# Kernel tuning notes

Measured on AMD Instinct MI355X. Metric: run time of the kernel, lower is better.

The kernel has to match this reference:

```python
import jax, jax.numpy as jnp
import numpy as np

B, CIN, H, W = 4, 256, 56, 56
COUT, K = 256, 3
STRIDE, PAD, OG = 1, 1, 1
KK = K * K


def setup_inputs() -> dict:
    key = jax.random.key(0)
    k1, k2, k3, k4 = jax.random.split(key, 4)
    x = jax.random.normal(k1, (B, CIN, H, W), jnp.float32)
    # deformable conv weight [Cout, Cin/groups, K, K]
    weight = jax.random.normal(k2, (COUT, CIN, K, K), jnp.float32) * 0.05
    # offset-predicting 3x3 conv: 2*OG*K*K output channels (small init -> modest offsets)
    off_w = jax.random.normal(k3, (2 * OG * KK, CIN, 3, 3), jnp.float32) * 0.01
    off_b = jax.random.normal(k4, (2 * OG * KK,), jnp.float32) * 0.01
    return {"x": x, "weight": weight, "off_w": off_w, "off_b": off_b}


def _deform_conv(x, weight, off_w, off_b):
    Bn, C, Hh, Ww = x.shape
    # offset = param_generator(x): 3x3 conv, stride 1, pad 1
    offset = jax.lax.conv_general_dilated(
        x, off_w, window_strides=(1, 1), padding=((1, 1), (1, 1)),
        dimension_numbers=("NCHW", "OIHW", "NCHW")) + off_b[None, :, None, None]
    Ho = (Hh + 2 * PAD - K) // STRIDE + 1
    Wo = (Ww + 2 * PAD - K) // STRIDE + 1
    # torchvision layout: [B, OG, KK, (dy,dx), Ho, Wo]
    off = offset.reshape(Bn, OG, KK, 2, Ho, Wo)

    kh = jnp.arange(KK) // K
    kw = jnp.arange(KK) % K
    base_y = (jnp.arange(Ho) * STRIDE - PAD)[None, :, None] + kh[:, None, None]  # [KK,Ho,1]
    base_x = (jnp.arange(Wo) * STRIDE - PAD)[None, None, :] + kw[:, None, None]  # [KK,1,Wo]
    py = base_y[None, None].astype(x.dtype) + off[:, :, :, 0]  # [B,OG,KK,Ho,Wo]
    px = base_x[None, None].astype(x.dtype) + off[:, :, :, 1]

    Cg = C // OG
    xg = x.reshape(Bn, OG, Cg, Hh * Ww)

    def gather(yc, xc, wgt):
        # zero-padded bilinear corner: out-of-bounds samples contribute 0
        valid = (yc >= 0) & (yc < Hh) & (xc >= 0) & (xc < Ww)
        idx = (jnp.clip(yc, 0, Hh - 1) * Ww + jnp.clip(xc, 0, Ww - 1)).reshape(Bn, OG, 1, -1)
        v = jnp.take_along_axis(xg, idx, axis=3)            # [B,OG,Cg,KK*Ho*Wo]
        w = (wgt * valid.astype(wgt.dtype)).reshape(Bn, OG, 1, -1)
        return v * w

    y0 = jnp.floor(py).astype(jnp.int32)
    x0 = jnp.floor(px).astype(jnp.int32)
    ty = py - y0
    tx = px - x0
    sampled = (gather(y0,     x0,     (1 - ty) * (1 - tx))
             + gather(y0,     x0 + 1, (1 - ty) * tx)
             + gather(y0 + 1, x0,     ty * (1 - tx))
             + gather(y0 + 1, x0 + 1, ty * tx))
    sampled = sampled.reshape(Bn, C, KK, Ho, Wo)
    # weighted accumulation: implicit GEMM over (Cin, KK)
    return jnp.einsum("bikhw,oik->bohw", sampled, weight.reshape(COUT, C, KK))


def reference(x, weight, off_w, off_b):
    return _deform_conv(x, weight, off_w, off_b)
```

## Files before the change

### kernel.cpp

```cpp
#include <hip/hip_runtime.h>
#include <hip/hip_bf16.h>

#define B_N   4
#define CIN_  256
#define HH_   56
#define WW_   56
#define COUT_ 256
#define KK_   9
#define HW_   3136
#define KDIM  2304
#define NOFF  (B_N*18*HW_)
#define NOUT  (B_N*COUT_*HW_)

typedef __attribute__((ext_vector_type(8))) short short8;
typedef __attribute__((ext_vector_type(4))) float float4v;

__device__ __forceinline__ short f2bf_bits(float v) {
    union { __hip_bfloat16 h; short s; } u;
    u.h = __float2bfloat16(v);
    return u.s;
}
__device__ __forceinline__ float bfbits2f(short s) {
    union { unsigned u; float f; } u2;
    u2.u = ((unsigned)(unsigned short)s) << 16;
    return u2.f;
}

#define NB_AT  2304
#define NB_XT  784
#define NB_OW3 288
__global__ __launch_bounds__(256) void k_front(const float* __restrict__ x,
                                               const float* __restrict__ wgt,
                                               const float* __restrict__ ow,
                                               short* __restrict__ At2,
                                               short* __restrict__ xTb,
                                               short* __restrict__ owT3) {
    __shared__ float tile[64][65];
    int bx = blockIdx.x;
    int t = threadIdx.x;
    if (bx < NB_AT) {
        int i = bx*256 + t;
        int e = i & 7;
        int l = (i >> 3) & 63;
        int gg = i >> 9;
        int g  = gg % 72;
        int rt = gg / 72;
        int m = rt*16 + (l & 15);
        int k = g*32 + (l >> 4)*8 + e;
        int kk = k >> 8;  int ci = k & 255;
        At2[i] = f2bf_bits(wgt[(size_t)(m*CIN_ + ci)*9 + kk]);
        return;
    }
    if (bx < NB_AT + NB_XT) {
        int g = bx - NB_AT;
        int b = g / 196; int r = g % 196;
        int c0 = (r / 49) * 64; int p0 = (r % 49) * 64;
        int tp = t & 63;  int tc = t >> 6;
        #pragma unroll
        for (int i = 0; i < 16; ++i) {
            int ci = tc*16 + i;
            tile[ci][tp] = x[((size_t)b*CIN_ + c0 + ci)*HW_ + p0 + tp];
        }
        __syncthreads();
        #pragma unroll
        for (int i = 0; i < 16; ++i) {
            int p = tc*16 + i;
            xTb[((size_t)b*HW_ + p0 + p)*CIN_ + c0 + tp] = f2bf_bits(tile[tp][p]);
        }
        return;
    }
    {
        int i = (bx - NB_AT - NB_XT)*256 + t;
        int c = i / KDIM; int r = i % KDIM;
        int kk = r >> 8;  int ci = r & 255;
        owT3[i] = (c < 18) ? f2bf_bits(ow[(size_t)(c*CIN_ + ci)*9 + kk]) : 0;
    }
}

__global__ __launch_bounds__(256) void k_offgemm(const short* __restrict__ owT3,
                                                 const short* __restrict__ xTb,
                                                 float* __restrict__ pOff2) {
    __shared__ short sA[32*64];
    __shared__ short sB[64*64];
    __shared__ int   sP2[64];
    int t = threadIdx.x;
    int posb = blockIdx.x * 64;
    int b    = blockIdx.y;
    int ks   = blockIdx.z;
    int kt0  = ks * 256;
    int kend = kt0 + 256;

    if (t < 64) {
        int pos = posb + t;
        int h = pos / WW_, w = pos % WW_;
        int yy = h + ks/3 - 1, xx = w + ks%3 - 1;
        bool v = (yy >= 0) && (yy < HH_) && (xx >= 0) && (xx < WW_);
        sP2[t] = v ? (yy*WW_ + xx) : -1;
    }
    __syncthreads();

    int arow = t >> 3,  aq  = t & 7;
    int brow = t >> 2,  bqc = (t & 3) * 2;

    int wv = t >> 6;
    int wm = (wv >> 1) * 16;
    int wn = (wv & 1) * 32;
    int lane = t & 63;
    int lm = lane & 15;
    int qd = lane >> 4;

    float4v acc[2];
    acc[0] = (float4v)(0.f); acc[1] = (float4v)(0.f);

    const short* gA = owT3 + (size_t)arow*KDIM + aq*8;
    const short* xb = xTb + (size_t)b*HW_*CIN_;

    short* wA = sA + (((arow >> 4)*8 + aq)*16 + ((arow + 2*aq) & 15))*8;
    short* wB[2];
    #pragma unroll
    for (int j = 0; j < 2; ++j) {
        int qq = bqc + j;
        wB[j] = sB + (((brow >> 4)*8 + qq)*16 + ((brow + 2*qq) & 15))*8;
    }

    short8 pa, pb[2];
    const short8 zero8 = (short8)(0);
    int p2 = sP2[brow];
    pa = *(const short8*)(gA + kt0);
    #pragma unroll
    for (int j = 0; j < 2; ++j) {
        int ci0 = (bqc + j)*8;
        pb[j] = (p2 >= 0) ? *(const short8*)(xb + (size_t)p2*CIN_ + ci0) : zero8;
    }

    for (int kt = kt0; kt < kend; kt += 64) {
        __syncthreads();
        *(short8*)wA = pa;
        #pragma unroll
        for (int j = 0; j < 2; ++j) *(short8*)wB[j] = pb[j];
        __syncthreads();
        int kt2 = kt + 64;
        if (kt2 < kend) {
            pa = *(const short8*)(gA + kt2);
            int cb = kt2 & 255;
            #pragma unroll
            for (int j = 0; j < 2; ++j) {
                int ci0 = cb + (bqc + j)*8;
                pb[j] = (p2 >= 0) ? *(const short8*)(xb + (size_t)p2*CIN_ + ci0) : zero8;
            }
        }
        #pragma unroll
        for (int kss = 0; kss < 2; ++kss) {
            int qe = kss*4 + qd;
            int sw = (lm + 2*qe) & 15;
            short8 af, bf[2];
            af = *(short8*)(sA + ((((wm>>4))*8 + qe)*16 + sw)*8);
            #pragma unroll
            for (int j = 0; j < 2; ++j)
                bf[j] = *(short8*)(sB + ((((wn>>4) + j)*8 + qe)*16 + sw)*8);
            #pragma unroll
            for (int j = 0; j < 2; ++j)
                acc[j] = __builtin_amdgcn_mfma_f32_16x16x32_bf16(
                             af, bf[j], acc[j], 0, 0, 0);
        }
    }

    float* pbase = pOff2 + (size_t)ks*NOFF;
    #pragma unroll
    for (int j = 0; j < 2; ++j) {
        int col = posb + wn + j*16 + lm;
        #pragma unroll
        for (int r = 0; r < 4; ++r) {
            int c = wm + qd*4 + r;
            if (c < 18)
                pbase[((size_t)(b*18 + c))*HW_ + col] = acc[j][r];
        }
    }
}

__global__ __launch_bounds__(256) void k_gemm(const short* __restrict__ At2,
                                              const short* __restrict__ xTb,
                                              const float* __restrict__ pOff2,
                                              const float* __restrict__ ob,
                                              float* __restrict__ pout) {
    __shared__ short sB[32*64];
    __shared__ int4   sPI[3*32];
    __shared__ float4 sPW[3*32];
    int t = threadIdx.x;

    int idx = blockIdx.x;
    int xcd = idx & 7;
    int b   = xcd & 3;
    int q   = (idx >> 3)*2 + (xcd >> 2);
    int sidx = q % 98;
    int ks   = q / 98;
    int posb = sidx * 32;

    for (int e = t; e < 3*32; e += 256) {
        int kk = ks*3 + (e >> 5); int pl = e & 31;
        int pos = posb + pl;
        int h = pos / WW_, w = pos % WW_;
        size_t oy = (size_t)(b*18 + 2*kk    )*HW_ + pos;
        size_t ox = (size_t)(b*18 + 2*kk + 1)*HW_ + pos;
        float dy = ob[2*kk], dx = ob[2*kk + 1];
        #pragma unroll
        for (int s = 0; s < 9; ++s) {
            dy += pOff2[(size_t)s*NOFF + oy];
            dx += pOff2[(size_t)s*NOFF + ox];
        }
        float py = (float)(h - 1 + kk/3) + dy;
        float px = (float)(w - 1 + kk%3) + dx;
        float y0f = floorf(py), x0f = floorf(px);
        int y0 = (int)y0f, x0 = (int)x0f;
        float ty = py - y0f, tx = px - x0f;
        bool vy0 = (y0   >= 0) && (y0   < HH_);
        bool vy1 = (y0+1 >= 0) && (y0+1 < HH_);
        bool vx0 = (x0   >= 0) && (x0   < WW_);
        bool vx1 = (x0+1 >= 0) && (x0+1 < WW_);
        int y0c = min(max(y0,   0), HH_-1), y1c = min(max(y0+1, 0), HH_-1);
        int x0c = min(max(x0,   0), WW_-1), x1c = min(max(x0+1, 0), WW_-1);
        sPI[e] = make_int4(y0c*WW_+x0c, y0c*WW_+x1c, y1c*WW_+x0c, y1c*WW_+x1c);
        sPW[e] = make_float4((vy0 && vx0) ? (1.f-ty)*(1.f-tx) : 0.f,
                             (vy0 && vx1) ? (1.f-ty)*tx       : 0.f,
                             (vy1 && vx0) ? ty*(1.f-tx)       : 0.f,
                             (vy1 && vx1) ? ty*tx             : 0.f);
    }
    __syncthreads();

    int brow = t >> 3;
    int bq   = t & 7;

    int wv = t >> 6;
    int lane = t & 63;
    int lm = lane & 15;
    int qd = lane >> 4;

    float4v acc[4][2];
    #pragma unroll
    for (int i = 0; i < 4; ++i)
        #pragma unroll
        for (int j = 0; j < 2; ++j) acc[i][j] = (float4v)(0.f);

    const short* xb = xTb + (size_t)b*HW_*CIN_;
    const short* pA = At2 + (((size_t)(wv*4) * 72) << 9) + (size_t)lane * 8;
    int g0 = ks * 24;

    short* wB = sB + (((brow >> 4)*8 + bq)*16 + ((brow + 2*bq) & 15))*8;

    short8 cg[4];
    float4 bwv;

#define CGLOAD(itX) do {                                                      \
    int4 id_ = sPI[((itX) >> 2)*32 + brow];                                   \
    bwv = sPW[((itX) >> 2)*32 + brow];                                        \
    int ci0_ = ((itX) & 3) * 64 + bq*8;                                       \
    cg[0] = *(const short8*)(xb + (size_t)id_.x*CIN_ + ci0_);                 \
    cg[1] = *(const short8*)(xb + (size_t)id_.y*CIN_ + ci0_);                 \
    cg[2] = *(const short8*)(xb + (size_t)id_.z*CIN_ + ci0_);                 \
    cg[3] = *(const short8*)(xb + (size_t)id_.w*CIN_ + ci0_);                 \
} while (0)

    CGLOAD(0);

    for (int it = 0; it < 12; ++it) {
        short8 af[8];
        #pragma unroll
        for (int kss = 0; kss < 2; ++kss)
            #pragma unroll
            for (int i = 0; i < 4; ++i)
                af[kss*4 + i] = *(const short8*)(
                    pA + ((size_t)(i*72 + g0 + it*2 + kss) << 9));

        short8 pk;
        {
            float f[8];
            #pragma unroll
            for (int e = 0; e < 8; ++e)
                f[e] = bwv.x*bfbits2f(cg[0][e]) + bwv.y*bfbits2f(cg[1][e])
                     + bwv.z*bfbits2f(cg[2][e]) + bwv.w*bfbits2f(cg[3][e]);
            union { short8 s8; __hip_bfloat162 h2[4]; } pu;
            #pragma unroll
            for (int e2 = 0; e2 < 4; ++e2)
                pu.h2[e2] = __float22bfloat162_rn(make_float2(f[2*e2], f[2*e2+1]));
            pk = pu.s8;
        }
        if (it + 1 < 12) CGLOAD(it + 1);

        __syncthreads();
        *(short8*)wB = pk;
        __syncthreads();

        #pragma unroll
        for (int kss = 0; kss < 2; ++kss) {
            int qe = kss*4 + qd;
            int sw = (lm + 2*qe) & 15;
            short8 bf[2];
            #pragma unroll
            for (int j = 0; j < 2; ++j)
                bf[j] = *(short8*)(sB + ((j*8 + qe)*16 + sw)*8);
            #pragma unroll
            for (int i = 0; i < 4; ++i)
                #pragma unroll
                for (int j = 0; j < 2; ++j)
                    acc[i][j] = __builtin_amdgcn_mfma_f32_16x16x32_bf16(
                                    af[kss*4 + i], bf[j], acc[i][j], 0, 0, 0);
        }
    }
#undef CGLOAD

    float* pbase = pout + (size_t)ks*NOUT;
    #pragma unroll
    for (int i = 0; i < 4; ++i)
        #pragma unroll
        for (int j = 0; j < 2; ++j) {
            int col = posb + j*16 + lm;
            #pragma unroll
            for (int r = 0; r < 4; ++r) {
                int m = wv*64 + i*16 + qd*4 + r;
                pbase[((size_t)b*COUT_ + m)*HW_ + col] = acc[i][j][r];
            }
        }
}

__global__ __launch_bounds__(256) void k_oreduce(const float* __restrict__ pout,
                                                 float* __restrict__ out) {
    int i = blockIdx.x*256 + threadIdx.x;
    if (i >= NOUT/4) return;
    float4 a = ((const float4*)pout)[i];
    float4 b = ((const float4*)(pout + NOUT))[i];
    float4 c = ((const float4*)(pout + 2*(size_t)NOUT))[i];
    float4 r;
    r.x = a.x + b.x + c.x;  r.y = a.y + b.y + c.y;
    r.z = a.z + b.z + c.z;  r.w = a.w + b.w + c.w;
    ((float4*)out)[i] = r;
}

extern "C" void kernel_launch(void* const* d_in, const int* in_sizes, int n_in,
                              void* d_out, int out_size, void* d_ws, size_t ws_size,
                              hipStream_t stream) {
    const float* x   = (const float*)d_in[0];
    const float* wgt = (const float*)d_in[1];
    const float* ow  = (const float*)d_in[2];
    const float* ob  = (const float*)d_in[3];
    float* out = (float*)d_out;

    char* ws = (char*)d_ws;
    short* At2   = (short*)ws;
    short* xTb   = (short*)(ws + 1179648);
    short* owT3  = (short*)(ws + 7602176);
    float* pOff2 = (float*)(ws + 7749632);
    float* pout  = (float*)(ws + 15878144);

    k_front  <<<dim3(NB_AT + NB_XT + NB_OW3), 256, 0, stream>>>(x, wgt, ow, At2, xTb, owT3);
    k_offgemm<<<dim3(49, 4, 9),               256, 0, stream>>>(owT3, xTb, pOff2);
    k_gemm   <<<dim3(1176),                   256, 0, stream>>>(At2, xTb, pOff2, ob, pout);
    k_oreduce<<<dim3(NOUT/4/256),             256, 0, stream>>>(pout, out);
}
```

Before: 121.6 us.

## Split bilinear sampling into separate im2col kernel feeding plain GEMM

Moves the offset-based bilinear gather and blend out of the GEMM main loop into a new kernel that materializes a bf16 sampled matrix in workspace. The GEMM then streams contiguous B tiles instead of doing four dependent gathers plus blend math per iteration. This removes gather latency from the MFMA loop, but adds a large intermediate buffer write and read plus an extra launch.

```diff
diff --git a/kernel.cpp b/kernel.cpp
--- a/kernel.cpp
+++ b/kernel.cpp
@@ -178,27 +178,19 @@
     }
 }
 
-__global__ __launch_bounds__(256) void k_gemm(const short* __restrict__ At2,
-                                              const short* __restrict__ xTb,
-                                              const float* __restrict__ pOff2,
-                                              const float* __restrict__ ob,
-                                              float* __restrict__ pout) {
-    __shared__ short sB[32*64];
-    __shared__ int4   sPI[3*32];
-    __shared__ float4 sPW[3*32];
+__global__ __launch_bounds__(256) void k_blend(const short* __restrict__ xTb,
+                                               const float* __restrict__ pOff2,
+                                               const float* __restrict__ ob,
+                                               short* __restrict__ xS) {
+    __shared__ int4   sPI[64];
+    __shared__ float4 sPW[64];
     int t = threadIdx.x;
-
-    int idx = blockIdx.x;
-    int xcd = idx & 7;
-    int b   = xcd & 3;
-    int q   = (idx >> 3)*2 + (xcd >> 2);
-    int sidx = q % 98;
-    int ks   = q / 98;
-    int posb = sidx * 32;
-
-    for (int e = t; e < 3*32; e += 256) {
-        int kk = ks*3 + (e >> 5); int pl = e & 31;
-        int pos = posb + pl;
+    int posb = blockIdx.x * 64;
+    int b    = blockIdx.y;
+    int kk   = blockIdx.z;
+
+    if (t < 64) {
+        int pos = posb + t;
         int h = pos / WW_, w = pos % WW_;
         size_t oy = (size_t)(b*18 + 2*kk    )*HW_ + pos;
         size_t ox = (size_t)(b*18 + 2*kk + 1)*HW_ + pos;
@@ -219,13 +211,54 @@
         bool vx1 = (x0+1 >= 0) && (x0+1 < WW_);
         int y0c = min(max(y0,   0), HH_-1), y1c = min(max(y0+1, 0), HH_-1);
         int x0c = min(max(x0,   0), WW_-1), x1c = min(max(x0+1, 0), WW_-1);
-        sPI[e] = make_int4(y0c*WW_+x0c, y0c*WW_+x1c, y1c*WW_+x0c, y1c*WW_+x1c);
-        sPW[e] = make_float4((vy0 && vx0) ? (1.f-ty)*(1.f-tx) : 0.f,
+        sPI[t] = make_int4(y0c*WW_+x0c, y0c*WW_+x1c, y1c*WW_+x0c, y1c*WW_+x1c);
+        sPW[t] = make_float4((vy0 && vx0) ? (1.f-ty)*(1.f-tx) : 0.f,
                              (vy0 && vx1) ? (1.f-ty)*tx       : 0.f,
                              (vy1 && vx0) ? ty*(1.f-tx)       : 0.f,
                              (vy1 && vx1) ? ty*tx             : 0.f);
     }
     __syncthreads();
+
+    const short* xb = xTb + (size_t)b*HW_*CIN_;
+    int ci0 = (t & 31) * 8;
+    int pl0 = t >> 5;
+    short* xo = xS + ((size_t)b*HW_ + posb)*KDIM + kk*256 + ci0;
+
+    #pragma unroll
+    for (int r = 0; r < 8; ++r) {
+        int pl = pl0 + r*8;
+        int4 id = sPI[pl]; float4 bwv = sPW[pl];
+        short8 c0 = *(const short8*)(xb + (size_t)id.x*CIN_ + ci0);
+        short8 c1 = *(const short8*)(xb + (size_t)id.y*CIN_ + ci0);
+        short8 c2 = *(const short8*)(xb + (size_t)id.z*CIN_ + ci0);
+        short8 c3 = *(const short8*)(xb + (size_t)id.w*CIN_ + ci0);
+        float f[8];
+        #pragma unroll
+        for (int e = 0; e < 8; ++e)
+            f[e] = bwv.x*bfbits2f(c0[e]) + bwv.y*bfbits2f(c1[e])
+                 + bwv.z*bfbits2f(c2[e]) + bwv.w*bfbits2f(c3[e]);
+        union { short8 s8; __hip_bfloat162 h2[4]; } pu;
+        #pragma unroll
+        for (int e2 = 0; e2 < 4; ++e2)
+            pu.h2[e2] = __float22bfloat162_rn(make_float2(f[2*e2], f[2*e2+1]));
+        *(short8*)(xo + (size_t)pl*KDIM) = pu.s8;
+    }
+}
+
+__global__ __launch_bounds__(256) void k_gemm(const short* __restrict__ At2,
+                                              const short* __restrict__ xS,
+                                              float* __restrict__ pout) {
+    __shared__ short sB[32*64];
+    int t = threadIdx.x;
+
+    int idx = blockIdx.x;
+    int xcd = idx & 7;
+    int b   = xcd & 3;
+    int q   = (idx >> 3)*2 + (xcd >> 2);
+    int sidx = q % 98;
+    int ks   = q / 98;
+    int posb = sidx * 32;
+    int kt0  = ks * 768;
 
     int brow = t >> 3;
     int bq   = t & 7;
@@ -241,26 +274,13 @@
         #pragma unroll
         for (int j = 0; j < 2; ++j) acc[i][j] = (float4v)(0.f);
 
-    const short* xb = xTb + (size_t)b*HW_*CIN_;
     const short* pA = At2 + (((size_t)(wv*4) * 72) << 9) + (size_t)lane * 8;
     int g0 = ks * 24;
 
+    const short* gB = xS + ((size_t)b*HW_ + posb + brow)*KDIM + kt0 + bq*8;
     short* wB = sB + (((brow >> 4)*8 + bq)*16 + ((brow + 2*bq) & 15))*8;
 
-    short8 cg[4];
-    float4 bwv;
-
-#define CGLOAD(itX) do {                                                      \
-    int4 id_ = sPI[((itX) >> 2)*32 + brow];                                   \
-    bwv = sPW[((itX) >> 2)*32 + brow];                                        \
-    int ci0_ = ((itX) & 3) * 64 + bq*8;                                       \
-    cg[0] = *(const short8*)(xb + (size_t)id_.x*CIN_ + ci0_);                 \
-    cg[1] = *(const short8*)(xb + (size_t)id_.y*CIN_ + ci0_);                 \
-    cg[2] = *(const short8*)(xb + (size_t)id_.z*CIN_ + ci0_);                 \
-    cg[3] = *(const short8*)(xb + (size_t)id_.w*CIN_ + ci0_);                 \
-} while (0)
-
-    CGLOAD(0);
+    short8 pb = *(const short8*)(gB);
 
     for (int it = 0; it < 12; ++it) {
         short8 af[8];
@@ -271,24 +291,11 @@
                 af[kss*4 + i] = *(const short8*)(
                     pA + ((size_t)(i*72 + g0 + it*2 + kss) << 9));
 
-        short8 pk;
-        {
-            float f[8];
-            #pragma unroll
-            for (int e = 0; e < 8; ++e)
-                f[e] = bwv.x*bfbits2f(cg[0][e]) + bwv.y*bfbits2f(cg[1][e])
-                     + bwv.z*bfbits2f(cg[2][e]) + bwv.w*bfbits2f(cg[3][e]);
-            union { short8 s8; __hip_bfloat162 h2[4]; } pu;
-            #pragma unroll
-            for (int e2 = 0; e2 < 4; ++e2)
-                pu.h2[e2] = __float22bfloat162_rn(make_float2(f[2*e2], f[2*e2+1]));
-            pk = pu.s8;
-        }
-        if (it + 1 < 12) CGLOAD(it + 1);
-
-        __syncthreads();
-        *(short8*)wB = pk;
-        __syncthreads();
+        __syncthreads();
+        *(short8*)wB = pb;
+        __syncthreads();
+        if (it + 1 < 12)
+            pb = *(const short8*)(gB + (it + 1)*64);
 
         #pragma unroll
         for (int kss = 0; kss < 2; ++kss) {
@@ -306,7 +313,6 @@
                                     af[kss*4 + i], bf[j], acc[i][j], 0, 0, 0);
         }
     }
-#undef CGLOAD
 
     float* pbase = pout + (size_t)ks*NOUT;
     #pragma unroll
@@ -349,10 +355,12 @@
     short* xTb   = (short*)(ws + 1179648);
     short* owT3  = (short*)(ws + 7602176);
     float* pOff2 = (float*)(ws + 7749632);
-    float* pout  = (float*)(ws + 15878144);
+    short* xS    = (short*)(ws + 15878144);
+    float* pout  = (float*)(ws + 73680896);
 
     k_front  <<<dim3(NB_AT + NB_XT + NB_OW3), 256, 0, stream>>>(x, wgt, ow, At2, xTb, owT3);
     k_offgemm<<<dim3(49, 4, 9),               256, 0, stream>>>(owT3, xTb, pOff2);
-    k_gemm   <<<dim3(1176),                   256, 0, stream>>>(At2, xTb, pOff2, ob, pout);
+    k_blend  <<<dim3(49, 4, 9),               256, 0, stream>>>(xTb, pOff2, ob, xS);
+    k_gemm   <<<dim3(1176),                   256, 0, stream>>>(At2, xS, pout);
     k_oreduce<<<dim3(NOUT/4/256),             256, 0, stream>>>(pout, out);
 }
```

Result: slower. 139.4 us (+14.7%).
